# Kernel optimization log

Hardware: AMD Instinct MI355X
Metric: run time of the kernel (lower is better)

## Reference

```python
import jax, jax.numpy as jnp
import numpy as np
import math

NO, NR, E = 100000, 1000, 1000000
DO, DR, DE, H, OM = 64, 32, 4, 64, 32


def setup_inputs() -> dict:
    key = jax.random.key(0)
    ks = jax.random.split(key, 20)
    s = lambda k, sh: jax.random.normal(k, sh, dtype=jnp.float32) * 0.05
    inp = {
        'x_order': jax.random.normal(ks[0], (NO, DO), dtype=jnp.float32),
        'x_rider': jax.random.normal(ks[1], (NR, DR), dtype=jnp.float32),
        'edge_attr': jax.random.normal(ks[2], (E, DE), dtype=jnp.float32),
        'order_idx': jax.random.randint(ks[3], (E,), 0, NO),
        'rider_idx': jax.random.randint(ks[4], (E,), 0, NR),
        'omega_encoded': jax.random.normal(ks[5], (OM,), dtype=jnp.float32),
        # TransformerConv params (heads=1)
        'Wk': s(ks[6], (DO, H)), 'bk': jnp.zeros((H,), jnp.float32),
        'Wq': s(ks[7], (DR, H)), 'bq': jnp.zeros((H,), jnp.float32),
        'Wv': s(ks[8], (DO, H)), 'bv': jnp.zeros((H,), jnp.float32),
        'We': s(ks[9], (DE, H)),  # lin_edge, bias=False in PyG
        'Wskip': s(ks[10], (DR, H)), 'bskip': jnp.zeros((H,), jnp.float32),
        # order_proj
        'Wp': s(ks[11], (DO, H)), 'bp': jnp.zeros((H,), jnp.float32),
        # residual MLP: Linear(2H+OM,128) -> ReLU -> Linear(128,1)
        'W1': s(ks[12], (2 * H + OM, 128)), 'b1': jnp.zeros((128,), jnp.float32),
        'W2': s(ks[13], (128, 1)), 'b2': jnp.zeros((1,), jnp.float32),
    }
    return inp


def _segment_softmax(alpha, seg, num_segments):
    m = jax.ops.segment_max(alpha, seg, num_segments=num_segments)
    m = jnp.where(jnp.isfinite(m), m, 0.0)
    ex = jnp.exp(alpha - m[seg])
    denom = jax.ops.segment_sum(ex, seg, num_segments=num_segments)
    return ex / (denom[seg] + 1e-16)


def reference(x_order, x_rider, edge_attr, order_idx, rider_idx, omega_encoded,
              Wk, bk, Wq, bq, Wv, bv, We, Wskip, bskip, Wp, bp, W1, b1, W2, b2):
    scale = 1.0 / math.sqrt(H)
    # TransformerConv((order, rider) -> rider), heads=1, edge_dim
    q = x_rider @ Wq + bq            # [NR, H]
    k = x_order @ Wk + bk            # [NO, H]
    v = x_order @ Wv + bv            # [NO, H]
    e = edge_attr @ We               # [E, H]
    k_j = k[order_idx] + e           # [E, H]
    v_j = v[order_idx] + e           # [E, H]
    alpha = jnp.sum(q[rider_idx] * k_j, axis=-1) * scale  # [E]
    alpha = _segment_softmax(alpha, rider_idx, NR)
    agg = jax.ops.segment_sum(alpha[:, None] * v_j, rider_idx, num_segments=NR)  # [NR, H]
    rider_emb = agg + x_rider @ Wskip + bskip  # root/skip connection

    # edge scoring
    order_proj = x_order @ Wp + bp   # [NO, H]
    oe = order_proj[order_idx]       # [E, H]
    re = rider_emb[rider_idx]        # [E, H]
    dot = jnp.sum(oe * re, axis=-1) * scale  # [E]
    omega_expand = jnp.broadcast_to(omega_encoded[None, :], (oe.shape[0], OM))
    resid_in = jnp.concatenate([oe, re, omega_expand], axis=-1)  # [E, 2H+OM]
    hmid = jax.nn.relu(resid_in @ W1 + b1)
    resid = (hmid @ W2 + b2)[:, 0]
    return jnp.clip(dot + resid, -10.0, 10.0)
```

## Files before the change

kernel.cpp:

```cpp
#include <hip/hip_runtime.h>
#include <hip/hip_bf16.h>
#include <math.h>
#include <stdint.h>

#define NO_N 100000
#define NR_N 1000
#define E_N  1000000
#define SB     250
#define SCHUNK 4000
#define KVP_TILES 1563
#define KVP_BLKS 1024
#define MAXTILES 17008

typedef short bf16x8 __attribute__((ext_vector_type(8)));
typedef float floatx4 __attribute__((ext_vector_type(4)));

__device__ __forceinline__ unsigned short bfu(float x) {
    union { __hip_bfloat16 h; unsigned short u; } c;
    c.h = __float2bfloat16(x);
    return c.u;
}
__device__ __forceinline__ float bflo(unsigned int u) {
    return __uint_as_float(u << 16);
}
__device__ __forceinline__ float bfhi(unsigned int u) {
    return __uint_as_float(u & 0xffff0000u);
}

__global__ __launch_bounds__(256) void k_front(
    const float* __restrict__ xr,
    const float* __restrict__ Wq, const float* __restrict__ bq,
    const float* __restrict__ Wskip, const float* __restrict__ bskip,
    const float* __restrict__ We,
    float* __restrict__ q, float* __restrict__ skip, float* __restrict__ t,
    const float* __restrict__ W1, const float* __restrict__ b1,
    const float* __restrict__ omega, float* __restrict__ b1eff,
    const float* __restrict__ x,
    const float* __restrict__ Wk, const float* __restrict__ bk,
    const float* __restrict__ Wv, const float* __restrict__ bv,
    const float* __restrict__ Wp, const float* __restrict__ bp,
    unsigned short* __restrict__ kb, unsigned short* __restrict__ vb,
    unsigned short* __restrict__ pb,
    const int* __restrict__ ridx, int* __restrict__ ghist)
{
    __shared__ __align__(16) char smem[9216];
    const int tid = threadIdx.x;
    const int b = blockIdx.x;

    if (b < 250) {
        float* sx = (float*)smem;
        float* sq = sx + 128;
        int rbase = b * 4;
        if (tid < 128) {
            int rl = tid >> 5, d = tid & 31;
            sx[rl * 32 + d] = xr[(rbase + rl) * 32 + d];
        }
        __syncthreads();
        int rl = tid >> 6, h = tid & 63;
        int r = rbase + rl;
        float aq = bq[h], as = bskip[h];
        #pragma unroll 4
        for (int d = 0; d < 32; ++d) {
            float xv = sx[rl * 32 + d];
            aq += xv * Wq[d * 64 + h];
            as += xv * Wskip[d * 64 + h];
        }
        sq[rl * 64 + h] = aq;
        q[r * 64 + h] = aq;
        skip[r * 64 + h] = as;
        __syncthreads();
        if (tid < 16) {
            int rl2 = tid >> 2, d = tid & 3;
            float acc = 0.f;
            for (int hh = 0; hh < 64; ++hh)
                acc += We[d * 64 + hh] * sq[rl2 * 64 + hh];
            t[(rbase + rl2) * 4 + d] = acc;
        }
    } else if (b == 250) {
        if (tid < 128) {
            float acc = b1[tid];
            #pragma unroll 4
            for (int j = 0; j < 32; ++j)
                acc += omega[j] * W1[(128 + j) * 128 + tid];
            b1eff[tid] = acc;
        }
    } else if (b < 251 + KVP_BLKS) {
        unsigned short* sX = (unsigned short*)smem;
        const int wave = tid >> 6, lane = tid & 63;
        const int l15 = lane & 15, quad = lane >> 4;

        bf16x8 bfr[3][2];
        float bias[3];
        unsigned short* outT[3];
        int colc[3];
        #pragma unroll
        for (int ct = 0; ct < 3; ++ct) {
            int n = wave * 48 + ct * 16 + l15;
            int table = n >> 6, c = n & 63;
            const float* W  = (table == 0) ? Wk : (table == 1) ? Wv : Wp;
            const float* bb = (table == 0) ? bk : (table == 1) ? bv : bp;
            bias[ct] = bb[c];
            colc[ct] = c;
            outT[ct] = (table == 0) ? kb : (table == 1) ? vb : pb;
            #pragma unroll
            for (int kf = 0; kf < 2; ++kf) {
                bf16x8 f;
                #pragma unroll
                for (int j = 0; j < 8; ++j)
                    f[j] = (short)bfu(W[(size_t)(kf * 32 + quad * 8 + j) * 64 + c]);
                bfr[ct][kf] = f;
            }
        }

        const int srl = tid >> 2;
        const int sqt = (tid & 3) * 16;

        for (int tile = b - 251; tile < KVP_TILES; tile += KVP_BLKS) {
            int rowbase = tile * 64;
            {
                int row = rowbase + srl;
                unsigned short* dst = sX + srl * 72 + sqt;
                if (row < NO_N) {
                    const float4* src = (const float4*)(x + (size_t)row * 64 + sqt);
                    #pragma unroll
                    for (int i = 0; i < 4; ++i) {
                        float4 a = src[i];
                        ushort4 u = { bfu(a.x), bfu(a.y), bfu(a.z), bfu(a.w) };
                        *(ushort4*)(dst + i * 4) = u;
                    }
                } else {
                    ushort4 z = {0, 0, 0, 0};
                    #pragma unroll
                    for (int i = 0; i < 4; ++i) *(ushort4*)(dst + i * 4) = z;
                }
            }
            __syncthreads();

            floatx4 acc[4][3];
            #pragma unroll
            for (int rt = 0; rt < 4; ++rt)
                #pragma unroll
                for (int ct = 0; ct < 3; ++ct)
                    acc[rt][ct] = (floatx4){bias[ct], bias[ct], bias[ct], bias[ct]};

            #pragma unroll
            for (int rt = 0; rt < 4; ++rt) {
                const unsigned short* ar = sX + (size_t)(rt * 16 + l15) * 72 + quad * 8;
                bf16x8 a0 = *(const bf16x8*)(ar);
                bf16x8 a1 = *(const bf16x8*)(ar + 32);
                #pragma unroll
                for (int ct = 0; ct < 3; ++ct) {
                    floatx4 c = acc[rt][ct];
                    c = __builtin_amdgcn_mfma_f32_16x16x32_bf16(a0, bfr[ct][0], c, 0, 0, 0);
                    c = __builtin_amdgcn_mfma_f32_16x16x32_bf16(a1, bfr[ct][1], c, 0, 0, 0);
                    acc[rt][ct] = c;
                }
            }

            #pragma unroll
            for (int rt = 0; rt < 4; ++rt) {
                int rb = rowbase + rt * 16 + quad * 4;
                #pragma unroll
                for (int ct = 0; ct < 3; ++ct) {
                    unsigned short* o = outT[ct];
                    size_t cbase = colc[ct];
                    #pragma unroll
                    for (int g = 0; g < 4; ++g) {
                        int row = rb + g;
                        if (row < NO_N)
                            o[(size_t)row * 64 + cbase] = bfu(acc[rt][ct][g]);
                    }
                }
            }
            __syncthreads();
        }
    } else {
        int* hc = (int*)smem;
        int hb = b - (251 + KVP_BLKS);
        for (int i = tid; i < NR_N; i += 256) hc[i] = 0;
        __syncthreads();
        int s = hb * SCHUNK;
        for (int i = s + tid; i < s + SCHUNK; i += 256)
            atomicAdd(&hc[ridx[i]], 1);
        __syncthreads();
        for (int i = tid; i < NR_N; i += 256)
            ghist[i * SB + hb] = hc[i];
    }
}

__global__ __launch_bounds__(256) void k_colscan(const int* __restrict__ ghist,
                                                 int* __restrict__ gpre,
                                                 int* __restrict__ counts)
{
    __shared__ int s[256];
    int tid = threadIdx.x, r = blockIdx.x;
    int v = (tid < SB) ? ghist[r * SB + tid] : 0;
    s[tid] = v;
    __syncthreads();
    for (int off = 1; off < 256; off <<= 1) {
        int tv = (tid >= off) ? s[tid - off] : 0;
        __syncthreads();
        s[tid] += tv;
        __syncthreads();
    }
    if (tid < SB) gpre[r * SB + tid] = s[tid] - v;
    if (tid == 255) counts[r] = s[255];
}

__global__ __launch_bounds__(1024) void k_scan(const int* __restrict__ counts,
                                               int* __restrict__ offsets,
                                               int* __restrict__ tilestart,
                                               int4* __restrict__ trec)
{
    __shared__ int s[1024];
    __shared__ int ofsL[NR_N];
    __shared__ int endL[NR_N];
    __shared__ int tsL[NR_N + 1];
    int tid = threadIdx.x;
    int c = (tid < NR_N) ? counts[tid] : 0;
    s[tid] = c;
    __syncthreads();
    for (int off = 1; off < 1024; off <<= 1) {
        int tv = (tid >= off) ? s[tid - off] : 0;
        __syncthreads();
        s[tid] += tv;
        __syncthreads();
    }
    int off0 = s[tid] - c;
    if (tid < NR_N) {
        offsets[tid] = off0;
        ofsL[tid] = off0;
        endL[tid] = off0 + c;
    }
    if (tid == NR_N - 1) offsets[NR_N] = s[tid];
    __syncthreads();
    int tc = (tid < NR_N) ? ((c + 63) >> 6) : 0;
    s[tid] = tc;
    __syncthreads();
    for (int off = 1; off < 1024; off <<= 1) {
        int tv = (tid >= off) ? s[tid - off] : 0;
        __syncthreads();
        s[tid] += tv;
        __syncthreads();
    }
    if (tid < NR_N) {
        int ts = s[tid] - tc;
        tsL[tid] = ts;
        tilestart[tid] = ts;
    }
    if (tid == NR_N - 1) {
        tsL[NR_N] = s[tid];
        tilestart[NR_N] = s[tid];
    }
    __syncthreads();
    int ntiles = tsL[NR_N];
    for (int t = tid; t < ntiles; t += 1024) {
        int lo = 0, hi = NR_N - 1;
        while (lo < hi) {
            int mid = (lo + hi + 1) >> 1;
            if (tsL[mid] <= t) lo = mid; else hi = mid - 1;
        }
        trec[t] = make_int4(lo, ofsL[lo] + ((t - tsL[lo]) << 6), endL[lo], 0);
    }
}

__global__ __launch_bounds__(256) void k_scatter2(
    const int* __restrict__ ridx, const int* __restrict__ oidx,
    const float* __restrict__ ea, const float* __restrict__ t,
    const int* __restrict__ offsets, const int* __restrict__ gpre,
    int4* __restrict__ spack, int* __restrict__ so, int* __restrict__ rank)
{
    __shared__ int cur[NR_N];
    int tid = threadIdx.x, b = blockIdx.x;
    for (int i = tid; i < NR_N; i += 256)
        cur[i] = offsets[i] + gpre[i * SB + b];
    __syncthreads();
    int s = b * SCHUNK;
    for (int i = s + tid; i < s + SCHUNK; i += 256) {
        int r = ridx[i];
        int o = oidx[i];
        float4 e4 = *(const float4*)(ea + (size_t)i * 4);
        float4 t4 = *(const float4*)(t + r * 4);
        float h = e4.x * t4.x + e4.y * t4.y + e4.z * t4.z + e4.w * t4.w;
        int pos = atomicAdd(&cur[r], 1);
        int4 pk;
        pk.x = o;
        pk.y = __float_as_int(h);
        pk.z = (int)((unsigned)bfu(e4.x) | ((unsigned)bfu(e4.y) << 16));
        pk.w = (int)((unsigned)bfu(e4.z) | ((unsigned)bfu(e4.w) << 16));
        spack[pos] = pk;
        so[pos] = o;
        rank[i] = pos;
    }
}

__global__ __launch_bounds__(512) void k_rider(
    const int* __restrict__ offsets, const int4* __restrict__ spack,
    const float* __restrict__ q,
    const unsigned short* __restrict__ kb, const unsigned short* __restrict__ vb,
    const float* __restrict__ We, const float* __restrict__ skip,
    const float* __restrict__ W1, const float* __restrict__ b1eff,
    float* __restrict__ emb, float* __restrict__ Br)
{
    __shared__ float sQ[64];
    __shared__ int2 sOX[8][64];
    __shared__ float rv[8][64];
    __shared__ float re4[8][4];
    __shared__ float rd[8];

    int r = blockIdx.x;
    int wave = threadIdx.x >> 6, lane = threadIdx.x & 63;
    if (threadIdx.x < 64) sQ[threadIdx.x] = q[r * 64 + threadIdx.x];
    __syncthreads();

    int beg = offsets[r], end = offsets[r + 1];
    int cnt = end - beg;
    int chunk = (cnt + 7) >> 3;
    int s0 = beg + wave * chunk;
    int s1 = min(s0 + chunk, end);

    float aggv = 0.f, dsum = 0.f;
    float ag0 = 0.f, ag1 = 0.f, ag2 = 0.f, ag3 = 0.f;
    const float2* sQ2 = (const float2*)sQ;

    for (int jb = s0; jb < s1; jb += 64) {
        int j = jb + lane;
        bool valid = (j < s1);
        int4 pk = make_int4(0, 0, 0, 0);
        if (valid) pk = spack[j];
        int oo = pk.x;
        float h = __int_as_float(pk.y);

        const uint4* krow = (const uint4*)(kb + (size_t)oo * 64);
        uint4 K0 = krow[0], K1 = krow[1], K2 = krow[2], K3 = krow[3];
        uint4 K4 = krow[4], K5 = krow[5], K6 = krow[6], K7 = krow[7];
        float acc = h;
        #define DOT8(Kv, base) { \
            float2 qa = sQ2[(base) + 0]; \
            acc = fmaf(bflo(Kv.x), qa.x, acc); acc = fmaf(bfhi(Kv.x), qa.y, acc); \
            float2 qb = sQ2[(base) + 1]; \
            acc = fmaf(bflo(Kv.y), qb.x, acc); acc = fmaf(bfhi(Kv.y), qb.y, acc); \
            float2 qc = sQ2[(base) + 2]; \
            acc = fmaf(bflo(Kv.z), qc.x, acc); acc = fmaf(bfhi(Kv.z), qc.y, acc); \
            float2 qd = sQ2[(base) + 3]; \
            acc = fmaf(bflo(Kv.w), qd.x, acc); acc = fmaf(bfhi(Kv.w), qd.y, acc); }
        DOT8(K0, 0) DOT8(K1, 4) DOT8(K2, 8) DOT8(K3, 12)
        DOT8(K4, 16) DOT8(K5, 20) DOT8(K6, 24) DOT8(K7, 28)
        #undef DOT8

        float exv = valid ? __expf(acc * 0.125f) : 0.f;
        dsum += exv;
        unsigned int ez = (unsigned int)pk.z, ew = (unsigned int)pk.w;
        ag0 = fmaf(exv, bflo(ez), ag0);
        ag1 = fmaf(exv, bfhi(ez), ag1);
        ag2 = fmaf(exv, bflo(ew), ag2);
        ag3 = fmaf(exv, bfhi(ew), ag3);

        sOX[wave][lane] = make_int2(oo, __float_as_int(exv));

        int nn = min(s1 - jb, 64);
        int i = 0;
        for (; i + 8 <= nn; i += 8) {
            int2 x0 = sOX[wave][i + 0], x1 = sOX[wave][i + 1];
            int2 x2 = sOX[wave][i + 2], x3 = sOX[wave][i + 3];
            int2 x4 = sOX[wave][i + 4], x5 = sOX[wave][i + 5];
            int2 x6 = sOX[wave][i + 6], x7 = sOX[wave][i + 7];
            unsigned short u0 = vb[(size_t)x0.x * 64 + lane];
            unsigned short u1 = vb[(size_t)x1.x * 64 + lane];
            unsigned short u2 = vb[(size_t)x2.x * 64 + lane];
            unsigned short u3 = vb[(size_t)x3.x * 64 + lane];
            unsigned short u4 = vb[(size_t)x4.x * 64 + lane];
            unsigned short u5 = vb[(size_t)x5.x * 64 + lane];
            unsigned short u6 = vb[(size_t)x6.x * 64 + lane];
            unsigned short u7 = vb[(size_t)x7.x * 64 + lane];
            aggv = fmaf(__int_as_float(x0.y), __uint_as_float((unsigned int)u0 << 16), aggv);
            aggv = fmaf(__int_as_float(x1.y), __uint_as_float((unsigned int)u1 << 16), aggv);
            aggv = fmaf(__int_as_float(x2.y), __uint_as_float((unsigned int)u2 << 16), aggv);
            aggv = fmaf(__int_as_float(x3.y), __uint_as_float((unsigned int)u3 << 16), aggv);
            aggv = fmaf(__int_as_float(x4.y), __uint_as_float((unsigned int)u4 << 16), aggv);
            aggv = fmaf(__int_as_float(x5.y), __uint_as_float((unsigned int)u5 << 16), aggv);
            aggv = fmaf(__int_as_float(x6.y), __uint_as_float((unsigned int)u6 << 16), aggv);
            aggv = fmaf(__int_as_float(x7.y), __uint_as_float((unsigned int)u7 << 16), aggv);
        }
        for (; i < nn; ++i) {
            int2 xx = sOX[wave][i];
            unsigned short uu = vb[(size_t)xx.x * 64 + lane];
            aggv = fmaf(__int_as_float(xx.y), __uint_as_float((unsigned int)uu << 16), aggv);
        }
    }

    #pragma unroll
    for (int m = 1; m < 64; m <<= 1) {
        dsum += __shfl_xor(dsum, m);
        ag0 += __shfl_xor(ag0, m);
        ag1 += __shfl_xor(ag1, m);
        ag2 += __shfl_xor(ag2, m);
        ag3 += __shfl_xor(ag3, m);
    }

    rv[wave][lane] = aggv;
    if (lane == 0) {
        rd[wave] = dsum;
        re4[wave][0] = ag0; re4[wave][1] = ag1;
        re4[wave][2] = ag2; re4[wave][3] = ag3;
    }
    __syncthreads();
    if (threadIdx.x < 64) {
        int l = threadIdx.x;
        float av = 0.f, ds = 0.f, a0 = 0.f, a1 = 0.f, a2 = 0.f, a3 = 0.f;
        #pragma unroll
        for (int w = 0; w < 8; ++w) {
            av += rv[w][l]; ds += rd[w];
            a0 += re4[w][0]; a1 += re4[w][1]; a2 += re4[w][2]; a3 += re4[w][3];
        }
        float corr = a0 * We[0 * 64 + l] + a1 * We[1 * 64 + l]
                   + a2 * We[2 * 64 + l] + a3 * We[3 * 64 + l];
        float val = (av + corr) / (ds + 1e-16f) + skip[r * 64 + l];
        emb[r * 64 + l] = val;
        sQ[l] = val;
    }
    __syncthreads();
    if (threadIdx.x < 128) {
        int c = threadIdx.x;
        float a = b1eff[c];
        #pragma unroll 8
        for (int d = 0; d < 64; ++d)
            a = fmaf(sQ[d], W1[(size_t)(64 + d) * 128 + c], a);
        Br[r * 128 + c] = a;
    }
}

__global__ __launch_bounds__(256) void k_edge2(
    const int* __restrict__ so, const int4* __restrict__ trec,
    const int* __restrict__ tilestart,
    const unsigned short* __restrict__ pb, const float* __restrict__ emb,
    const float* __restrict__ Br, const float* __restrict__ W1,
    const float* __restrict__ W2, const float* __restrict__ b2,
    float* __restrict__ tmp)
{
    __shared__ __align__(16) unsigned short sW[128 * 72];

    const int tid = threadIdx.x;
    const int wave = tid >> 6;
    const int lane = tid & 63;
    const int l15 = lane & 15;
    const int quad = lane >> 4;

    for (int idx = tid; idx < 64 * 128; idx += 256) {
        int k = idx >> 7, n = idx & 127;
        sW[n * 72 + k] = bfu(W1[idx]);
    }
    __syncthreads();

    bf16x8 bfr[8][2];
    float w2v[8];
    #pragma unroll
    for (int ctl = 0; ctl < 8; ++ctl) {
        int n = ctl * 16 + l15;
        w2v[ctl] = W2[n];
        #pragma unroll
        for (int kc = 0; kc < 2; ++kc)
            bfr[ctl][kc] = *(const bf16x8*)(sW + n * 72 + kc * 32 + quad * 8);
    }
    float b2v = b2[0];
    const int ntiles = tilestart[NR_N];

    union U4B { uint4 u; bf16x8 b; };

    for (int tile = blockIdx.x * 4 + wave; tile < ntiles; tile += gridDim.x * 4) {
        int4 rr = trec[tile];
        const int r = rr.x, jb = rr.y, jend = rr.z;

        int o_l = so[min(jb + lane, jend - 1)];
        U4B A0[4], A1[4];
        #pragma unroll
        for (int rt = 0; rt < 4; ++rt) {
            int osrc = __shfl(o_l, rt * 16 + l15);
            const unsigned short* rowp = pb + (size_t)osrc * 64 + quad * 8;
            A0[rt].u = *(const uint4*)(rowp);
            A1[rt].u = *(const uint4*)(rowp + 32);
        }

        const float* er = emb + r * 64;
        float dotv[4];
        #pragma unroll
        for (int rt = 0; rt < 4; ++rt) {
            const float* e0 = er + quad * 8;
            const float* e1 = er + 32 + quad * 8;
            float d = 0.f;
            d = fmaf(bflo(A0[rt].u.x), e0[0], d); d = fmaf(bfhi(A0[rt].u.x), e0[1], d);
            d = fmaf(bflo(A0[rt].u.y), e0[2], d); d = fmaf(bfhi(A0[rt].u.y), e0[3], d);
            d = fmaf(bflo(A0[rt].u.z), e0[4], d); d = fmaf(bfhi(A0[rt].u.z), e0[5], d);
            d = fmaf(bflo(A0[rt].u.w), e0[6], d); d = fmaf(bfhi(A0[rt].u.w), e0[7], d);
            d = fmaf(bflo(A1[rt].u.x), e1[0], d); d = fmaf(bfhi(A1[rt].u.x), e1[1], d);
            d = fmaf(bflo(A1[rt].u.y), e1[2], d); d = fmaf(bfhi(A1[rt].u.y), e1[3], d);
            d = fmaf(bflo(A1[rt].u.z), e1[4], d); d = fmaf(bfhi(A1[rt].u.z), e1[5], d);
            d = fmaf(bflo(A1[rt].u.w), e1[6], d); d = fmaf(bfhi(A1[rt].u.w), e1[7], d);
            d += __shfl_xor(d, 16);
            d += __shfl_xor(d, 32);
            dotv[rt] = d;
        }

        float brv[8];
        #pragma unroll
        for (int ctl = 0; ctl < 8; ++ctl)
            brv[ctl] = Br[r * 128 + ctl * 16 + l15];

        #pragma unroll
        for (int rt = 0; rt < 4; ++rt) {
            floatx4 s = (floatx4){0.f, 0.f, 0.f, 0.f};
            #pragma unroll
            for (int ctl = 0; ctl < 8; ++ctl) {
                floatx4 c = (floatx4){0.f, 0.f, 0.f, 0.f};
                c = __builtin_amdgcn_mfma_f32_16x16x32_bf16(A0[rt].b, bfr[ctl][0], c, 0, 0, 0);
                c = __builtin_amdgcn_mfma_f32_16x16x32_bf16(A1[rt].b, bfr[ctl][1], c, 0, 0, 0);
                #pragma unroll
                for (int g = 0; g < 4; ++g)
                    s[g] = fmaf(fmaxf(c[g] + brv[ctl], 0.f), w2v[ctl], s[g]);
            }
            #pragma unroll
            for (int m = 1; m < 16; m <<= 1) {
                s[0] += __shfl_xor(s[0], m);
                s[1] += __shfl_xor(s[1], m);
                s[2] += __shfl_xor(s[2], m);
                s[3] += __shfl_xor(s[3], m);
            }
            float sd0 = __shfl(dotv[rt], quad * 4 + 0);
            float sd1 = __shfl(dotv[rt], quad * 4 + 1);
            float sd2 = __shfl(dotv[rt], quad * 4 + 2);
            float sd3 = __shfl(dotv[rt], quad * 4 + 3);
            if (l15 == 0) {
                int rowb = rt * 16 + quad * 4;
                float sdv[4] = { sd0, sd1, sd2, sd3 };
                #pragma unroll
                for (int g = 0; g < 4; ++g) {
                    int pos = jb + rowb + g;
                    if (pos < jend) {
                        float v = s[g] + 0.125f * sdv[g] + b2v;
                        tmp[pos] = fminf(fmaxf(v, -10.f), 10.f);
                    }
                }
            }
        }
    }
}

__global__ __launch_bounds__(256) void k_perm(const int* __restrict__ rank,
                                              const float* __restrict__ tmp,
                                              float* __restrict__ out)
{
    int i = blockIdx.x * 256 + threadIdx.x;
    if (i < E_N) out[i] = tmp[rank[i]];
}

extern "C" void kernel_launch(void* const* d_in, const int* in_sizes, int n_in,
                              void* d_out, int out_size, void* d_ws, size_t ws_size,
                              hipStream_t stream)
{
    const float* x_order   = (const float*)d_in[0];
    const float* x_rider   = (const float*)d_in[1];
    const float* edge_attr = (const float*)d_in[2];
    const int*   order_idx = (const int*)d_in[3];
    const int*   rider_idx = (const int*)d_in[4];
    const float* omega     = (const float*)d_in[5];
    const float* Wk = (const float*)d_in[6];  const float* bk = (const float*)d_in[7];
    const float* Wq = (const float*)d_in[8];  const float* bq = (const float*)d_in[9];
    const float* Wv = (const float*)d_in[10]; const float* bv = (const float*)d_in[11];
    const float* We = (const float*)d_in[12];
    const float* Wskip = (const float*)d_in[13]; const float* bskip = (const float*)d_in[14];
    const float* Wp = (const float*)d_in[15]; const float* bp = (const float*)d_in[16];
    const float* W1 = (const float*)d_in[17]; const float* b1 = (const float*)d_in[18];
    const float* W2 = (const float*)d_in[19]; const float* b2 = (const float*)d_in[20];
    float* out = (float*)d_out;

    unsigned short* ws_kb = (unsigned short*)d_ws;
    unsigned short* ws_vb = ws_kb + (size_t)NO_N * 64;
    unsigned short* ws_pb = ws_vb + (size_t)NO_N * 64;
    int4* ws_spack = (int4*)(ws_pb + (size_t)NO_N * 64);
    float* ws_tmp  = (float*)ws_spack;
    int*  ws_so    = (int*)(ws_spack + E_N);
    int*  ws_rank  = ws_so + E_N;
    float* wsf     = (float*)(ws_rank + E_N);
    float* ws_q    = wsf;
    float* ws_skip = ws_q + NR_N * 64;
    float* ws_emb  = ws_skip + NR_N * 64;
    float* ws_t    = ws_emb + NR_N * 64;
    float* ws_b1e  = ws_t + NR_N * 4;
    float* ws_Br   = ws_b1e + 128;
    int* ws_counts  = (int*)(ws_Br + NR_N * 128);
    int* ws_offsets = ws_counts + NR_N;
    int* ws_tilest  = ws_offsets + NR_N + 8;
    int* ws_ghist   = ws_tilest + NR_N + 8;
    int* ws_gpre    = ws_ghist + NR_N * SB;
    int4* ws_trec   = (int4*)(((uintptr_t)(ws_gpre + NR_N * SB) + 15) & ~(uintptr_t)15);

    k_front<<<251 + KVP_BLKS + SB, 256, 0, stream>>>(
        x_rider, Wq, bq, Wskip, bskip, We, ws_q, ws_skip, ws_t,
        W1, b1, omega, ws_b1e,
        x_order, Wk, bk, Wv, bv, Wp, bp, ws_kb, ws_vb, ws_pb,
        rider_idx, ws_ghist);
    k_colscan<<<NR_N, 256, 0, stream>>>(ws_ghist, ws_gpre, ws_counts);
    k_scan<<<1, 1024, 0, stream>>>(ws_counts, ws_offsets, ws_tilest, ws_trec);
    k_scatter2<<<SB, 256, 0, stream>>>(rider_idx, order_idx, edge_attr, ws_t,
                                       ws_offsets, ws_gpre, ws_spack, ws_so, ws_rank);
    k_rider<<<NR_N, 512, 0, stream>>>(ws_offsets, ws_spack, ws_q,
                                      ws_kb, ws_vb, We, ws_skip,
                                      W1, ws_b1e, ws_emb, ws_Br);
    k_edge2<<<1024, 256, 0, stream>>>(ws_so, ws_trec, ws_tilest,
                                      ws_pb, ws_emb, ws_Br, W1, W2, b2, ws_tmp);
    k_perm<<<(E_N + 255) / 256, 256, 0, stream>>>(ws_rank, ws_tmp, out);
}
```

Measured before the change: 301.5 us.

## Compute edge dot product via MFMA with bf16 rider embedding; parallelize tile records

The per-edge dot product between the order projection and the rider embedding moves from scalar FMAs plus shuffles onto two extra bf16 MFMA instructions. The B operand is the rider embedding, now stored as bf16, placed only in column 0. The tile-record construction also moves out of the single-block scan kernel into its own multi-block kernel, which removes a serial binary-search loop at the cost of one extra launch. Storing the embedding in bf16 lowers precision of the dot term, and most of each MFMA's work is wasted on zero columns.

```diff
diff --git a/kernel.cpp b/kernel.cpp
--- a/kernel.cpp
+++ b/kernel.cpp
@@ -209,13 +209,9 @@
 
 __global__ __launch_bounds__(1024) void k_scan(const int* __restrict__ counts,
                                                int* __restrict__ offsets,
-                                               int* __restrict__ tilestart,
-                                               int4* __restrict__ trec)
+                                               int* __restrict__ tilestart)
 {
     __shared__ int s[1024];
-    __shared__ int ofsL[NR_N];
-    __shared__ int endL[NR_N];
-    __shared__ int tsL[NR_N + 1];
     int tid = threadIdx.x;
     int c = (tid < NR_N) ? counts[tid] : 0;
     s[tid] = c;
@@ -226,12 +222,7 @@
         s[tid] += tv;
         __syncthreads();
     }
-    int off0 = s[tid] - c;
-    if (tid < NR_N) {
-        offsets[tid] = off0;
-        ofsL[tid] = off0;
-        endL[tid] = off0 + c;
-    }
+    if (tid < NR_N) offsets[tid] = s[tid] - c;
     if (tid == NR_N - 1) offsets[NR_N] = s[tid];
     __syncthreads();
     int tc = (tid < NR_N) ? ((c + 63) >> 6) : 0;
@@ -243,25 +234,24 @@
         s[tid] += tv;
         __syncthreads();
     }
-    if (tid < NR_N) {
-        int ts = s[tid] - tc;
-        tsL[tid] = ts;
-        tilestart[tid] = ts;
-    }
-    if (tid == NR_N - 1) {
-        tsL[NR_N] = s[tid];
-        tilestart[NR_N] = s[tid];
-    }
-    __syncthreads();
-    int ntiles = tsL[NR_N];
-    for (int t = tid; t < ntiles; t += 1024) {
-        int lo = 0, hi = NR_N - 1;
-        while (lo < hi) {
-            int mid = (lo + hi + 1) >> 1;
-            if (tsL[mid] <= t) lo = mid; else hi = mid - 1;
-        }
-        trec[t] = make_int4(lo, ofsL[lo] + ((t - tsL[lo]) << 6), endL[lo], 0);
-    }
+    if (tid < NR_N) tilestart[tid] = s[tid] - tc;
+    if (tid == NR_N - 1) tilestart[NR_N] = s[tid];
+}
+
+__global__ __launch_bounds__(256) void k_trec(const int* __restrict__ tilestart,
+                                              const int* __restrict__ offsets,
+                                              int4* __restrict__ trec)
+{
+    int nt = tilestart[NR_N];
+    int t = blockIdx.x * 256 + threadIdx.x;
+    if (t >= nt) return;
+    int lo = 0, hi = NR_N - 1;
+    while (lo < hi) {
+        int mid = (lo + hi + 1) >> 1;
+        if (tilestart[mid] <= t) lo = mid; else hi = mid - 1;
+    }
+    trec[t] = make_int4(lo, offsets[lo] + ((t - tilestart[lo]) << 6),
+                        offsets[lo + 1], 0);
 }
 
 __global__ __launch_bounds__(256) void k_scatter2(
@@ -300,7 +290,7 @@
     const unsigned short* __restrict__ kb, const unsigned short* __restrict__ vb,
     const float* __restrict__ We, const float* __restrict__ skip,
     const float* __restrict__ W1, const float* __restrict__ b1eff,
-    float* __restrict__ emb, float* __restrict__ Br)
+    unsigned short* __restrict__ embb, float* __restrict__ Br)
 {
     __shared__ float sQ[64];
     __shared__ int2 sOX[8][64];
@@ -416,7 +406,7 @@
         float corr = a0 * We[0 * 64 + l] + a1 * We[1 * 64 + l]
                    + a2 * We[2 * 64 + l] + a3 * We[3 * 64 + l];
         float val = (av + corr) / (ds + 1e-16f) + skip[r * 64 + l];
-        emb[r * 64 + l] = val;
+        embb[r * 64 + l] = bfu(val);
         sQ[l] = val;
     }
     __syncthreads();
@@ -433,7 +423,7 @@
 __global__ __launch_bounds__(256) void k_edge2(
     const int* __restrict__ so, const int4* __restrict__ trec,
     const int* __restrict__ tilestart,
-    const unsigned short* __restrict__ pb, const float* __restrict__ emb,
+    const unsigned short* __restrict__ pb, const unsigned short* __restrict__ embb,
     const float* __restrict__ Br, const float* __restrict__ W1,
     const float* __restrict__ W2, const float* __restrict__ b2,
     float* __restrict__ tmp)
@@ -464,6 +454,7 @@
     }
     float b2v = b2[0];
     const int ntiles = tilestart[NR_N];
+    const bf16x8 z8 = (bf16x8){0, 0, 0, 0, 0, 0, 0, 0};
 
     union U4B { uint4 u; bf16x8 b; };
 
@@ -481,25 +472,11 @@
             A1[rt].u = *(const uint4*)(rowp + 32);
         }
 
-        const float* er = emb + r * 64;
-        float dotv[4];
-        #pragma unroll
-        for (int rt = 0; rt < 4; ++rt) {
-            const float* e0 = er + quad * 8;
-            const float* e1 = er + 32 + quad * 8;
-            float d = 0.f;
-            d = fmaf(bflo(A0[rt].u.x), e0[0], d); d = fmaf(bfhi(A0[rt].u.x), e0[1], d);
-            d = fmaf(bflo(A0[rt].u.y), e0[2], d); d = fmaf(bfhi(A0[rt].u.y), e0[3], d);
-            d = fmaf(bflo(A0[rt].u.z), e0[4], d); d = fmaf(bfhi(A0[rt].u.z), e0[5], d);
-            d = fmaf(bflo(A0[rt].u.w), e0[6], d); d = fmaf(bfhi(A0[rt].u.w), e0[7], d);
-            d = fmaf(bflo(A1[rt].u.x), e1[0], d); d = fmaf(bfhi(A1[rt].u.x), e1[1], d);
-            d = fmaf(bflo(A1[rt].u.y), e1[2], d); d = fmaf(bfhi(A1[rt].u.y), e1[3], d);
-            d = fmaf(bflo(A1[rt].u.z), e1[4], d); d = fmaf(bfhi(A1[rt].u.z), e1[5], d);
-            d = fmaf(bflo(A1[rt].u.w), e1[6], d); d = fmaf(bfhi(A1[rt].u.w), e1[7], d);
-            d += __shfl_xor(d, 16);
-            d += __shfl_xor(d, 32);
-            dotv[rt] = d;
-        }
+        const unsigned short* eb = embb + r * 64;
+        bf16x8 e0 = *(const bf16x8*)(eb + quad * 8);
+        bf16x8 e1 = *(const bf16x8*)(eb + 32 + quad * 8);
+        bf16x8 b80 = z8, b81 = z8;
+        if (l15 == 0) { b80 = e0; b81 = e1; }
 
         float brv[8];
         #pragma unroll
@@ -518,6 +495,10 @@
                 for (int g = 0; g < 4; ++g)
                     s[g] = fmaf(fmaxf(c[g] + brv[ctl], 0.f), w2v[ctl], s[g]);
             }
+            floatx4 c8 = (floatx4){0.f, 0.f, 0.f, 0.f};
+            c8 = __builtin_amdgcn_mfma_f32_16x16x32_bf16(A0[rt].b, b80, c8, 0, 0, 0);
+            c8 = __builtin_amdgcn_mfma_f32_16x16x32_bf16(A1[rt].b, b81, c8, 0, 0, 0);
+
             #pragma unroll
             for (int m = 1; m < 16; m <<= 1) {
                 s[0] += __shfl_xor(s[0], m);
@@ -525,18 +506,13 @@
                 s[2] += __shfl_xor(s[2], m);
                 s[3] += __shfl_xor(s[3], m);
             }
-            float sd0 = __shfl(dotv[rt], quad * 4 + 0);
-            float sd1 = __shfl(dotv[rt], quad * 4 + 1);
-            float sd2 = __shfl(dotv[rt], quad * 4 + 2);
-            float sd3 = __shfl(dotv[rt], quad * 4 + 3);
             if (l15 == 0) {
                 int rowb = rt * 16 + quad * 4;
-                float sdv[4] = { sd0, sd1, sd2, sd3 };
                 #pragma unroll
                 for (int g = 0; g < 4; ++g) {
                     int pos = jb + rowb + g;
                     if (pos < jend) {
-                        float v = s[g] + 0.125f * sdv[g] + b2v;
+                        float v = s[g] + 0.125f * c8[g] + b2v;
                         tmp[pos] = fminf(fmaxf(v, -10.f), 10.f);
                     }
                 }
@@ -583,8 +559,8 @@
     float* wsf     = (float*)(ws_rank + E_N);
     float* ws_q    = wsf;
     float* ws_skip = ws_q + NR_N * 64;
-    float* ws_emb  = ws_skip + NR_N * 64;
-    float* ws_t    = ws_emb + NR_N * 64;
+    unsigned short* ws_embb = (unsigned short*)(ws_skip + NR_N * 64);
+    float* ws_t    = (float*)(ws_embb + NR_N * 64);
     float* ws_b1e  = ws_t + NR_N * 4;
     float* ws_Br   = ws_b1e + 128;
     int* ws_counts  = (int*)(ws_Br + NR_N * 128);
@@ -600,13 +576,14 @@
         x_order, Wk, bk, Wv, bv, Wp, bp, ws_kb, ws_vb, ws_pb,
         rider_idx, ws_ghist);
     k_colscan<<<NR_N, 256, 0, stream>>>(ws_ghist, ws_gpre, ws_counts);
-    k_scan<<<1, 1024, 0, stream>>>(ws_counts, ws_offsets, ws_tilest, ws_trec);
+    k_scan<<<1, 1024, 0, stream>>>(ws_counts, ws_offsets, ws_tilest);
+    k_trec<<<(MAXTILES + 255) / 256, 256, 0, stream>>>(ws_tilest, ws_offsets, ws_trec);
     k_scatter2<<<SB, 256, 0, stream>>>(rider_idx, order_idx, edge_attr, ws_t,
                                        ws_offsets, ws_gpre, ws_spack, ws_so, ws_rank);
     k_rider<<<NR_N, 512, 0, stream>>>(ws_offsets, ws_spack, ws_q,
                                       ws_kb, ws_vb, We, ws_skip,
-                                      W1, ws_b1e, ws_emb, ws_Br);
+                                      W1, ws_b1e, ws_embb, ws_Br);
     k_edge2<<<1024, 256, 0, stream>>>(ws_so, ws_trec, ws_tilest,
-                                      ws_pb, ws_emb, ws_Br, W1, W2, b2, ws_tmp);
+                                      ws_pb, ws_embb, ws_Br, W1, W2, b2, ws_tmp);
     k_perm<<<(E_N + 255) / 256, 256, 0, stream>>>(ws_rank, ws_tmp, out);
 }
```

Result: faster. 287.8 us (-4.6%).
